# Kernel optimization log

Measured on AMD Instinct MI355X. Metric: run time of the kernel, lower is better.

The kernel has to match this reference:

```python
import jax, jax.numpy as jnp
import numpy as np

VOCAB, EMBED, MAXLEN, UNITS, F1, BATCH = 50000, 256, 512, 32, 16, 512

def setup_inputs() -> dict:
    key = jax.random.key(0)
    ks = jax.random.split(key, 9)
    tokens = jax.random.randint(ks[0], (BATCH, MAXLEN), 0, VOCAB, dtype=jnp.int32)
    emb_table = jax.random.normal(ks[1], (VOCAB, EMBED), dtype=jnp.float32) * 0.02
    # SimpleRNN params (Keras: kernel, recurrent_kernel, bias)
    Wx = jax.random.normal(ks[2], (EMBED, UNITS), dtype=jnp.float32) * (1.0 / np.sqrt(EMBED))
    Wh = jax.random.normal(ks[3], (UNITS, UNITS), dtype=jnp.float32) * (1.0 / np.sqrt(UNITS))
    b  = jnp.zeros((UNITS,), dtype=jnp.float32)
    W1 = jax.random.normal(ks[4], (UNITS, F1), dtype=jnp.float32) * (1.0 / np.sqrt(UNITS))
    b1 = jnp.zeros((F1,), dtype=jnp.float32)
    W2 = jax.random.normal(ks[5], (F1, 1), dtype=jnp.float32) * (1.0 / np.sqrt(F1))
    b2 = jnp.zeros((1,), dtype=jnp.float32)
    return {"tokens": tokens, "emb_table": emb_table, "Wx": Wx, "Wh": Wh, "b": b,
            "W1": W1, "b1": b1, "W2": W2, "b2": b2}

def reference(tokens, emb_table, Wx, Wh, b, W1, b1, W2, b2):
    # Embedding lookup: [B, T, E]
    x = emb_table[tokens]
    # SimpleRNN recurrence (tanh), return last hidden state. Dropout disabled (inference).
    xs = jnp.transpose(x, (1, 0, 2))  # time-major [T, B, E]
    h0 = jnp.zeros((tokens.shape[0], Wh.shape[0]), dtype=x.dtype)

    def step(h, x_t):
        h_new = jnp.tanh(x_t @ Wx + h @ Wh + b)
        return h_new, None

    h_last, _ = jax.lax.scan(step, h0, xs)
    # Flatten is a no-op on [B, 32]; Dense heads are linear (no activation), then sigmoid.
    z = (h_last @ W1 + b1) @ W2 + b2
    return jax.nn.sigmoid(z)  # [B, 1]
```

## Files before the change

### kernel.cpp

```cpp
#include <hip/hip_runtime.h>
#include <hip/hip_bf16.h>
#include <math.h>

#define TT 512
#define BB 512
#define EE 256
#define UU 32
#define FF1 16
#define NWAVE 2048

#define TWO_LOG2E 2.8853900817779268f

__device__ __forceinline__ float rdlane(float v, int lane) {
    return __int_as_float(__builtin_amdgcn_readlane(__float_as_int(v), lane));
}

#define DPP_ADD(v, ctrl)                                                    \
    (v) += __int_as_float(__builtin_amdgcn_update_dpp(                      \
        0, __float_as_int(v), (ctrl), 0xf, 0xf, true))

__global__ __launch_bounds__(64) void proj_dpp(
    const float* __restrict__ emb, const float* __restrict__ Wx,
    const float* __restrict__ bias, float* __restrict__ P, int nrows)
{
    const int L = threadIdx.x;
    const int g = L >> 4;
    const int c = L & 15;
    const int wv = blockIdx.x;

    float w[8][2][8];
    #pragma unroll
    for (int kk = 0; kk < 8; ++kk) {
        #pragma unroll
        for (int d = 0; d < 2; ++d) {
            const int row = 32 * kk + 2 * c + d;
            const float4* src = (const float4*)(Wx + (size_t)row * UU + g * 8);
            float4 a = src[0], b = src[1];
            w[kk][d][0] = a.x; w[kk][d][1] = a.y; w[kk][d][2] = a.z; w[kk][d][3] = a.w;
            w[kk][d][4] = b.x; w[kk][d][5] = b.y; w[kk][d][6] = b.z; w[kk][d][7] = b.w;
        }
    }
    float bs[8];
    #pragma unroll
    for (int uu = 0; uu < 8; ++uu) bs[uu] = bias[g * 8 + uu];

    auto rowptr2 = [&](int i) {
        int r = wv + NWAVE * i;
        if (r >= nrows) r = nrows - 1;
        return (const float2*)(emb + (size_t)r * EE);
    };

    float2 xA[8], xB[8];
    {
        const float2* rp = rowptr2(0);
        #pragma unroll
        for (int kk = 0; kk < 8; ++kk) xA[kk] = rp[kk * 16 + c];
    }

    const int NI = (nrows - 1 - wv) / NWAVE + 1;

    for (int i = 0; i < NI; ++i) {
        {
            const float2* rp = rowptr2(i + 1 < NI ? i + 1 : i);
            #pragma unroll
            for (int kk = 0; kk < 8; ++kk) xB[kk] = rp[kk * 16 + c];
        }

        float p[8];
        #pragma unroll
        for (int uu = 0; uu < 8; ++uu) p[uu] = 0.f;
        #pragma unroll
        for (int kk = 0; kk < 8; ++kk) {
            const float2 xp = xA[kk];
            #pragma unroll
            for (int uu = 0; uu < 8; ++uu)
                p[uu] = fmaf(xp.x, w[kk][0][uu], p[uu]);
            #pragma unroll
            for (int uu = 0; uu < 8; ++uu)
                p[uu] = fmaf(xp.y, w[kk][1][uu], p[uu]);
        }

        #pragma unroll
        for (int uu = 0; uu < 8; ++uu) {
            DPP_ADD(p[uu], 0x111);
            DPP_ADD(p[uu], 0x112);
            DPP_ADD(p[uu], 0x114);
            DPP_ADD(p[uu], 0x118);
        }

        if (c == 15) {
            const int r = wv + NWAVE * i;
            float4 o0, o1;
            o0.x = (p[0] + bs[0]) * TWO_LOG2E;
            o0.y = (p[1] + bs[1]) * TWO_LOG2E;
            o0.z = (p[2] + bs[2]) * TWO_LOG2E;
            o0.w = (p[3] + bs[3]) * TWO_LOG2E;
            o1.x = (p[4] + bs[4]) * TWO_LOG2E;
            o1.y = (p[5] + bs[5]) * TWO_LOG2E;
            o1.z = (p[6] + bs[6]) * TWO_LOG2E;
            o1.w = (p[7] + bs[7]) * TWO_LOG2E;
            float4* dst = (float4*)(P + (size_t)r * UU + g * 8);
            dst[0] = o0; dst[1] = o1;
        }

        #pragma unroll
        for (int kk = 0; kk < 8; ++kk) xA[kk] = xB[kk];
    }
}

__global__ __launch_bounds__(64) void scan_heads(
    const int* __restrict__ tokens, const float* __restrict__ P,
    const float* __restrict__ Wh,
    const float* __restrict__ W1, const float* __restrict__ b1,
    const float* __restrict__ W2, const float* __restrict__ b2,
    float* __restrict__ out)
{
    __shared__ float xs[TT * UU];

    const int L = threadIdx.x;
    const int u = L & 31;
    const int b = blockIdx.x;
    const int* trow = tokens + b * TT;

    float wr[UU];
    float S = 0.f;
    #pragma unroll
    for (int k = 0; k < UU; ++k) {
        float whk = Wh[k * UU + u] * TWO_LOG2E;
        S += whk;
        wr[k] = -2.0f * whk;
    }

    const int sub = L >> 3;
    const int q   = L & 7;
    for (int c = 0; c < 8; ++c) {
        int tk8[8];
        #pragma unroll
        for (int i = 0; i < 8; ++i)
            tk8[i] = trow[c * 64 + i * 8 + sub];
        #pragma unroll
        for (int i = 0; i < 8; ++i) {
            const float* src = P + (size_t)tk8[i] * UU + q * 4;
            float* dst = xs + (c * 64 + i * 8) * UU;
            __builtin_amdgcn_global_load_lds(
                (const __attribute__((address_space(1))) void*)src,
                (__attribute__((address_space(3))) void*)dst, 16, 0, 0);
        }
    }
    __syncthreads();

    if (L < 32) {
        float xA[8], xB[8];
        #pragma unroll
        for (int j = 0; j < 8; ++j) xA[j] = xs[j * UU + u] + S;

        float r = 0.5f;

        auto step = [&](float rc, float x) -> float {
            float rv[UU];
            #pragma unroll
            for (int k = 0; k < UU; ++k) rv[k] = rdlane(rc, k);

            float a0 = fmaf(rv[0], wr[0], x);
            float a1 = rv[1] * wr[1];
            float a2 = rv[2] * wr[2];
            float a3 = rv[3] * wr[3];
            #pragma unroll
            for (int k = 4; k < UU; k += 4) {
                a0 = fmaf(rv[k],     wr[k],     a0);
                a1 = fmaf(rv[k + 1], wr[k + 1], a1);
                a2 = fmaf(rv[k + 2], wr[k + 2], a2);
                a3 = fmaf(rv[k + 3], wr[k + 3], a3);
            }
            float e = __builtin_amdgcn_exp2f((a0 + a1) + (a2 + a3));
            return __builtin_amdgcn_rcpf(e + 1.0f);
        };

        for (int t = 0; t < TT; t += 16) {
            #pragma unroll
            for (int j = 0; j < 8; ++j)
                xB[j] = xs[((t + 8 + j) & (TT - 1)) * UU + u] + S;
            #pragma unroll
            for (int j = 0; j < 8; ++j) r = step(r, xA[j]);
            #pragma unroll
            for (int j = 0; j < 8; ++j)
                xA[j] = xs[((t + 16 + j) & (TT - 1)) * UU + u] + S;
            #pragma unroll
            for (int j = 0; j < 8; ++j) r = step(r, xB[j]);
        }

        float h = fmaf(-2.0f, r, 1.0f);

        const int j = L & 15;
        float s = b1[j];
        #pragma unroll
        for (int k = 0; k < UU; ++k) {
            float hk = rdlane(h, k);
            s = fmaf(hk, W1[k * FF1 + j], s);
        }
        float z = b2[0];
        #pragma unroll
        for (int jj = 0; jj < FF1; ++jj) {
            float yj = rdlane(s, jj);
            z = fmaf(yj, W2[jj], z);
        }
        if (L == 0) {
            float e = __builtin_amdgcn_exp2f(-z * 1.4426950408889634f);
            out[b] = __builtin_amdgcn_rcpf(1.0f + e);
        }
    }
}

extern "C" void kernel_launch(void* const* d_in, const int* in_sizes, int n_in,
                              void* d_out, int out_size, void* d_ws, size_t ws_size,
                              hipStream_t stream) {
    const int*   tokens = (const int*)  d_in[0];
    const float* emb    = (const float*)d_in[1];
    const float* Wx     = (const float*)d_in[2];
    const float* Wh     = (const float*)d_in[3];
    const float* bias   = (const float*)d_in[4];
    const float* W1     = (const float*)d_in[5];
    const float* b1     = (const float*)d_in[6];
    const float* W2     = (const float*)d_in[7];
    const float* b2     = (const float*)d_in[8];
    float* out = (float*)d_out;

    const int vocab = in_sizes[1] / EE;
    float* P = (float*)d_ws;

    proj_dpp<<<dim3(NWAVE), dim3(64), 0, stream>>>(
        emb, Wx, bias, P, vocab);

    scan_heads<<<dim3(BB), dim3(64), 0, stream>>>(
        tokens, P, Wh, W1, b1, W2, b2, out);
}
```

Measured before the change: 189.9 us.

## Double projection grid, widen recurrence accumulators, drop half-wave scan guard

The vocabulary projection kernel now launches 4096 single-wave blocks instead of 2048, with an early exit for blocks past the vocab size, to give more parallelism to the bandwidth-bound projection. The recurrence step uses eight independent FMA accumulator chains instead of four, to shorten the dependent FMA chain on the serial critical path. The L<32 guard is removed so all 64 lanes run the scan uniformly, which avoids the divergence branch but has the upper lanes do redundant work. The double-buffered x prefetch is simplified into a single 8-step lookahead.

Result: no change. 191.0 us (+0.6%).

```diff
diff --git a/kernel.cpp b/kernel.cpp
--- a/kernel.cpp
+++ b/kernel.cpp
@@ -7,7 +7,7 @@
 #define EE 256
 #define UU 32
 #define FF1 16
-#define NWAVE 2048
+#define NWAVE 4096
 
 #define TWO_LOG2E 2.8853900817779268f
 
@@ -27,6 +27,8 @@
     const int g = L >> 4;
     const int c = L & 15;
     const int wv = blockIdx.x;
+
+    if (wv >= nrows) return;
 
     float w[8][2][8];
     #pragma unroll
@@ -149,65 +151,68 @@
     }
     __syncthreads();
 
-    if (L < 32) {
-        float xA[8], xB[8];
-        #pragma unroll
-        for (int j = 0; j < 8; ++j) xA[j] = xs[j * UU + u] + S;
-
-        float r = 0.5f;
-
-        auto step = [&](float rc, float x) -> float {
+    float xr[8];
+    #pragma unroll
+    for (int j = 0; j < 8; ++j) xr[j] = xs[j * UU + u] + S;
+
+    float r = 0.5f;
+
+    for (int t = 0; t < TT; t += 8) {
+        float xn[8];
+        #pragma unroll
+        for (int j = 0; j < 8; ++j)
+            xn[j] = xs[((t + 8 + j) & (TT - 1)) * UU + u] + S;
+
+        #pragma unroll
+        for (int j = 0; j < 8; ++j) {
             float rv[UU];
             #pragma unroll
-            for (int k = 0; k < UU; ++k) rv[k] = rdlane(rc, k);
-
-            float a0 = fmaf(rv[0], wr[0], x);
+            for (int k = 0; k < UU; ++k) rv[k] = rdlane(r, k);
+
+            float a0 = fmaf(rv[0], wr[0], xr[j]);
             float a1 = rv[1] * wr[1];
             float a2 = rv[2] * wr[2];
             float a3 = rv[3] * wr[3];
-            #pragma unroll
-            for (int k = 4; k < UU; k += 4) {
+            float a4 = rv[4] * wr[4];
+            float a5 = rv[5] * wr[5];
+            float a6 = rv[6] * wr[6];
+            float a7 = rv[7] * wr[7];
+            #pragma unroll
+            for (int k = 8; k < UU; k += 8) {
                 a0 = fmaf(rv[k],     wr[k],     a0);
                 a1 = fmaf(rv[k + 1], wr[k + 1], a1);
                 a2 = fmaf(rv[k + 2], wr[k + 2], a2);
                 a3 = fmaf(rv[k + 3], wr[k + 3], a3);
+                a4 = fmaf(rv[k + 4], wr[k + 4], a4);
+                a5 = fmaf(rv[k + 5], wr[k + 5], a5);
+                a6 = fmaf(rv[k + 6], wr[k + 6], a6);
+                a7 = fmaf(rv[k + 7], wr[k + 7], a7);
             }
-            float e = __builtin_amdgcn_exp2f((a0 + a1) + (a2 + a3));
-            return __builtin_amdgcn_rcpf(e + 1.0f);
-        };
-
-        for (int t = 0; t < TT; t += 16) {
-            #pragma unroll
-            for (int j = 0; j < 8; ++j)
-                xB[j] = xs[((t + 8 + j) & (TT - 1)) * UU + u] + S;
-            #pragma unroll
-            for (int j = 0; j < 8; ++j) r = step(r, xA[j]);
-            #pragma unroll
-            for (int j = 0; j < 8; ++j)
-                xA[j] = xs[((t + 16 + j) & (TT - 1)) * UU + u] + S;
-            #pragma unroll
-            for (int j = 0; j < 8; ++j) r = step(r, xB[j]);
-        }
-
-        float h = fmaf(-2.0f, r, 1.0f);
-
-        const int j = L & 15;
-        float s = b1[j];
-        #pragma unroll
-        for (int k = 0; k < UU; ++k) {
-            float hk = rdlane(h, k);
-            s = fmaf(hk, W1[k * FF1 + j], s);
-        }
-        float z = b2[0];
-        #pragma unroll
-        for (int jj = 0; jj < FF1; ++jj) {
-            float yj = rdlane(s, jj);
-            z = fmaf(yj, W2[jj], z);
-        }
-        if (L == 0) {
-            float e = __builtin_amdgcn_exp2f(-z * 1.4426950408889634f);
-            out[b] = __builtin_amdgcn_rcpf(1.0f + e);
-        }
+            float s01 = a0 + a1, s23 = a2 + a3, s45 = a4 + a5, s67 = a6 + a7;
+            float e = __builtin_amdgcn_exp2f((s01 + s23) + (s45 + s67));
+            r = __builtin_amdgcn_rcpf(e + 1.0f);
+            xr[j] = xn[j];
+        }
+    }
+
+    float h = fmaf(-2.0f, r, 1.0f);
+
+    const int j = threadIdx.x & 15;
+    float s = b1[j];
+    #pragma unroll
+    for (int k = 0; k < UU; ++k) {
+        float hk = rdlane(h, k);
+        s = fmaf(hk, W1[k * FF1 + j], s);
+    }
+    float z = b2[0];
+    #pragma unroll
+    for (int jj = 0; jj < FF1; ++jj) {
+        float yj = rdlane(s, jj);
+        z = fmaf(yj, W2[jj], z);
+    }
+    if (threadIdx.x == 0) {
+        float e = __builtin_amdgcn_exp2f(-z * 1.4426950408889634f);
+        out[b] = __builtin_amdgcn_rcpf(1.0f + e);
     }
 }
 
```
